# Kernel optimization log

Measured on AMD Instinct MI355X. Metric: run time of the kernel, lower is better.

Reference implementation:

```python
import jax, jax.numpy as jnp
import numpy as np

B, C, H, W = 4, 256, 128, 128
D = 256            # attention hidden_dim (== C, so no output_proj)
HID = 1024         # mlp hidden = int(C * 4.0)
EPS = 1e-5


def setup_inputs() -> dict:
    key = jax.random.key(0)
    ks = jax.random.split(key, 16)
    s = 0.02
    return {
        "x": jax.random.normal(ks[0], (B, C, H, W), jnp.float32),
        "wq": jax.random.normal(ks[1], (C, D), jnp.float32) * s,
        "bq": jnp.zeros((D,), jnp.float32),
        "wk": jax.random.normal(ks[2], (C, D), jnp.float32) * s,
        "bk": jnp.zeros((D,), jnp.float32),
        "wv": jax.random.normal(ks[3], (C, D), jnp.float32) * s,
        "bv": jnp.zeros((D,), jnp.float32),
        "ln1_g": jnp.ones((C,), jnp.float32),
        "ln1_b": jnp.zeros((C,), jnp.float32),
        "ln2_g": jnp.ones((C,), jnp.float32),
        "ln2_b": jnp.zeros((C,), jnp.float32),
        "fc1_w": jax.random.normal(ks[4], (C, HID), jnp.float32) * s,
        "fc1_b": jnp.zeros((HID,), jnp.float32),
        "fc2_w": jax.random.normal(ks[5], (HID, C), jnp.float32) * s,
        "fc2_b": jnp.zeros((C,), jnp.float32),
    }


def _layernorm(x, g, b):
    m = jnp.mean(x, axis=-1, keepdims=True)
    v = jnp.mean(jnp.square(x - m), axis=-1, keepdims=True)
    return (x - m) * jax.lax.rsqrt(v + EPS) * g + b


def _neighborhoods(t):
    # t: [B,H,W,D] -> [B,H,W,9,D] 3x3 neighborhoods, zero-padded at borders
    tp = jnp.pad(t, ((0, 0), (1, 1), (1, 1), (0, 0)))
    h, w = t.shape[1], t.shape[2]
    return jnp.stack(
        [tp[:, dy:dy + h, dx:dx + w, :] for dy in range(3) for dx in range(3)],
        axis=3,
    )


def _valid_mask(h, w):
    # [H,W,9] bool: which of the 9 neighbors are inside the grid
    ys = jnp.arange(h)[:, None] * jnp.ones((1, w), jnp.int32)
    xs = jnp.arange(w)[None, :] * jnp.ones((h, 1), jnp.int32)
    top, bot = ys > 0, ys < h - 1
    lef, rig = xs > 0, xs < w - 1
    ones = jnp.ones((h, w), bool)
    return jnp.stack(
        [top & lef, top, top & rig, lef, ones, rig, bot & lef, bot, bot & rig],
        axis=-1,
    )


def reference(x, wq, bq, wk, bk, wv, bv, ln1_g, ln1_b, ln2_g, ln2_b,
              fc1_w, fc1_b, fc2_w, fc2_b):
    b_, c_, h_, w_ = x.shape
    xc = jnp.transpose(x, (0, 2, 3, 1))                    # [B,H,W,C]
    n1 = _layernorm(xc, ln1_g, ln1_b)
    q = n1 @ wq + bq                                       # [B,H,W,D]
    k = n1 @ wk + bk
    v = n1 @ wv + bv
    kn = _neighborhoods(k)                                  # [B,H,W,9,D]
    vn = _neighborhoods(v)
    scores = jnp.einsum('bhwd,bhwnd->bhwn', q, kn) / jnp.sqrt(jnp.float32(q.shape[-1]))
    mask = _valid_mask(h_, w_)                               # [H,W,9]
    scores = jnp.where(mask, scores, jnp.float32(-1e9))
    weights = jax.nn.softmax(scores, axis=-1)
    attn = jnp.einsum('bhwn,bhwnd->bhwd', weights, vn)       # [B,H,W,D]
    x1 = xc + attn                                           # residual 1
    n2 = _layernorm(x1, ln2_g, ln2_b)
    mlp = jax.nn.gelu(n2 @ fc1_w + fc1_b, approximate=False) @ fc2_w + fc2_b
    out = x1 + mlp
    return jnp.transpose(out, (0, 3, 1, 2))                  # [B,C,H,W]
```

## Files before the change

### kernel.cpp

```cpp
#include <hip/hip_runtime.h>
#include <hip/hip_bf16.h>
#include <math.h>

#define NPIX  65536
#define CCH   256
#define HWSZ  16384
#define WIDTH 128
#define HID   1024

typedef unsigned short u16;
typedef __bf16 bf16x8 __attribute__((ext_vector_type(8)));
typedef float  floatx4 __attribute__((ext_vector_type(4)));

__device__ __forceinline__ float bf2f(u16 u) {
  union { unsigned int i; float f; } c; c.i = ((unsigned int)u) << 16; return c.f;
}
__device__ __forceinline__ float bflo(unsigned int u) {
  union { unsigned int i; float f; } c; c.i = u << 16; return c.f;
}
__device__ __forceinline__ float bfhi(unsigned int u) {
  union { unsigned int i; float f; } c; c.i = u & 0xffff0000u; return c.f;
}
__device__ __forceinline__ u16 f2bf(float f) {
  union { float f; unsigned int i; } c; c.f = f;
  unsigned int x = c.i;
  x += 0x7fffu + ((x >> 16) & 1u);
  return (u16)(x >> 16);
}
__device__ __forceinline__ unsigned int packbf(float lo, float hi) {
  return ((unsigned int)f2bf(hi) << 16) | (unsigned int)f2bf(lo);
}
__device__ __forceinline__ float fast_rcp(float x) {
  float r; asm("v_rcp_f32 %0, %1" : "=v"(r) : "v"(x)); return r;
}
__device__ __forceinline__ float fast_exp2(float x) {
  float r; asm("v_exp_f32 %0, %1" : "=v"(r) : "v"(x)); return r;
}
__device__ __forceinline__ float gelu_fast(float x) {
  const float u = x * x;
  const float s = x * fmaf(0.1029432f, u, 2.3022082f);
  const float e = fast_exp2(-s);
  return x * fast_rcp(1.0f + e);
}

__device__ __forceinline__ void async16(const void* g, void* l) {
  __builtin_amdgcn_global_load_lds(
      (const __attribute__((address_space(1))) void*)g,
      (__attribute__((address_space(3))) void*)l, 16, 0, 0);
}

__global__ __launch_bounds__(256) void wfrag_kernel(
    const float* __restrict__ src, u16* __restrict__ dst, int N, int K) {
  const int tid = threadIdx.x;
  const int u = blockIdx.x * 4 + (tid >> 6);
  const int lane = tid & 63, quad = lane >> 4, l16 = lane & 15;
  const int K32 = K >> 5;
  const int g = u / K32, kb = u - g * K32;
  const int n = g * 16 + l16;
  const int k0 = kb * 32 + quad * 8;
  u16 tmp[8];
#pragma unroll
  for (int e = 0; e < 8; e++) tmp[e] = f2bf(src[(size_t)(k0 + e) * N + n]);
  *(bf16x8*)(dst + ((size_t)u * 64 + lane) * 8) = *(bf16x8*)tmp;
}

__global__ __launch_bounds__(256) void concat_bias_kernel(
    const float* __restrict__ bq, const float* __restrict__ bk,
    const float* __restrict__ bv, float* __restrict__ dst) {
  const int i = blockIdx.x * 256 + threadIdx.x;
  if (i < 256) dst[i] = bq[i];
  else if (i < 512) dst[i] = bk[i - 256];
  else if (i < 768) dst[i] = bv[i - 512];
}

__global__ __launch_bounds__(256) void ln1_kernel(
    const float* __restrict__ x, const float* __restrict__ g,
    const float* __restrict__ bb, u16* __restrict__ n1) {
  __shared__ float sx[32][257];
  __shared__ float sred[16][32];
  __shared__ float sm[32], sr[32];
  const int tx = threadIdx.x;
  const int p0 = blockIdx.x * 32;
  {
    const int pix = tx & 31, cpart = tx >> 5;
    const int p = p0 + pix;
    const int b = p >> 14, hw = p & (HWSZ - 1);
    const float* xb = x + ((size_t)b * CCH) * HWSZ + hw;
    float s = 0.f, s2 = 0.f;
#pragma unroll 4
    for (int i = 0; i < 32; i++) {
      const int c = cpart * 32 + i;
      const float v = xb[(size_t)c * HWSZ];
      sx[pix][c] = v;
      s += v; s2 += v * v;
    }
    sred[cpart][pix] = s; sred[8 + cpart][pix] = s2;
  }
  __syncthreads();
  if (tx < 32) {
    float s = 0.f, s2 = 0.f;
#pragma unroll
    for (int j = 0; j < 8; j++) { s += sred[j][tx]; s2 += sred[8 + j][tx]; }
    const float m = s * (1.0f / 256.0f);
    const float var = s2 * (1.0f / 256.0f) - m * m;
    sm[tx] = m; sr[tx] = rsqrtf(var + 1e-5f);
  }
  __syncthreads();
  const float gc = g[tx], bc = bb[tx];
#pragma unroll 4
  for (int i = 0; i < 32; i++) {
    const float v = (sx[i][tx] - sm[i]) * sr[i] * gc + bc;
    n1[(size_t)(p0 + i) * CCH + tx] = f2bf(v);
  }
}

__global__ __launch_bounds__(256) void res_ln2_kernel(
    const float* __restrict__ x, const u16* __restrict__ attn,
    const float* __restrict__ g, const float* __restrict__ bb,
    float* __restrict__ x1, u16* __restrict__ n2) {
  __shared__ float sx[32][257];
  __shared__ float sred[16][32];
  __shared__ float sm[32], sr[32];
  const int tx = threadIdx.x;
  const int p0 = blockIdx.x * 32;
  {
    const int pix = tx & 31, cpart = tx >> 5;
    const int p = p0 + pix;
    const int b = p >> 14, hw = p & (HWSZ - 1);
    const float* xb = x + ((size_t)b * CCH) * HWSZ + hw;
#pragma unroll 4
    for (int i = 0; i < 32; i++) {
      const int c = cpart * 32 + i;
      sx[pix][c] = xb[(size_t)c * HWSZ];
    }
  }
  __syncthreads();
#pragma unroll 4
  for (int i = 0; i < 32; i++) {
    const float v = sx[i][tx] + bf2f(attn[(size_t)(p0 + i) * CCH + tx]);
    sx[i][tx] = v;
    x1[(size_t)(p0 + i) * CCH + tx] = v;
  }
  __syncthreads();
  {
    const int pix = tx & 31, cpart = tx >> 5;
    float s = 0.f, s2 = 0.f;
#pragma unroll 4
    for (int i = 0; i < 32; i++) {
      const float v = sx[pix][cpart * 32 + i];
      s += v; s2 += v * v;
    }
    sred[cpart][pix] = s; sred[8 + cpart][pix] = s2;
  }
  __syncthreads();
  if (tx < 32) {
    float s = 0.f, s2 = 0.f;
#pragma unroll
    for (int j = 0; j < 8; j++) { s += sred[j][tx]; s2 += sred[8 + j][tx]; }
    const float m = s * (1.0f / 256.0f);
    const float var = s2 * (1.0f / 256.0f) - m * m;
    sm[tx] = m; sr[tx] = rsqrtf(var + 1e-5f);
  }
  __syncthreads();
  const float gc = g[tx], bc = bb[tx];
#pragma unroll 4
  for (int i = 0; i < 32; i++) {
    const float v = (sx[i][tx] - sm[i]) * sr[i] * gc + bc;
    n2[(size_t)(p0 + i) * CCH + tx] = f2bf(v);
  }
}

__global__ __launch_bounds__(256) void attn_kernel(
    const u16* __restrict__ qkv, u16* __restrict__ attn) {
  const int tid = threadIdx.x;
  const int wave = tid >> 6, lane = tid & 63;
  const int p = blockIdx.x * 4 + wave;
  const int hw = p & (HWSZ - 1);
  const int hh = hw >> 7, ww = hw & (WIDTH - 1);
  const u16* rowp = qkv + (size_t)p * 768 + lane * 4;
  const uint2 qr = *(const uint2*)rowp;
  const float qf0 = bflo(qr.x), qf1 = bfhi(qr.x);
  const float qf2 = bflo(qr.y), qf3 = bfhi(qr.y);
  float sc[9];
#pragma unroll
  for (int n = 0; n < 9; n++) {
    const int dy = n / 3 - 1, dx = n % 3 - 1;
    const int y = hh + dy, x2 = ww + dx;
    float s = -1e30f;
    if (y >= 0 && y < 128 && x2 >= 0 && x2 < 128) {
      const uint2 kr = *(const uint2*)(rowp + 256 + (dy * WIDTH + dx) * 768);
      float d = qf0 * bflo(kr.x) + qf1 * bfhi(kr.x)
              + qf2 * bflo(kr.y) + qf3 * bfhi(kr.y);
#pragma unroll
      for (int o = 32; o >= 1; o >>= 1) d += __shfl_xor(d, o, 64);
      s = d * 0.0625f;
    }
    sc[n] = s;
  }
  float mx = sc[0];
#pragma unroll
  for (int n = 1; n < 9; n++) mx = fmaxf(mx, sc[n]);
  float wgt[9], wsum = 0.f;
#pragma unroll
  for (int n = 0; n < 9; n++) { wgt[n] = __expf(sc[n] - mx); wsum += wgt[n]; }
  const float inv = 1.0f / wsum;
  float a0 = 0.f, a1 = 0.f, a2 = 0.f, a3 = 0.f;
#pragma unroll
  for (int n = 0; n < 9; n++) {
    const int dy = n / 3 - 1, dx = n % 3 - 1;
    const int y = hh + dy, x2 = ww + dx;
    if (y >= 0 && y < 128 && x2 >= 0 && x2 < 128) {
      const uint2 vr = *(const uint2*)(rowp + 512 + (dy * WIDTH + dx) * 768);
      const float wn = wgt[n] * inv;
      a0 += wn * bflo(vr.x); a1 += wn * bfhi(vr.x);
      a2 += wn * bflo(vr.y); a3 += wn * bfhi(vr.y);
    }
  }
  uint2 o;
  o.x = ((unsigned int)f2bf(a1) << 16) | (unsigned int)f2bf(a0);
  o.y = ((unsigned int)f2bf(a3) << 16) | (unsigned int)f2bf(a2);
  *(uint2*)(attn + (size_t)p * CCH + lane * 4) = o;
}

template <int NCH, int NST, int EPI>
__global__ __launch_bounds__(256, 3) void gemm_blds(
    const u16* __restrict__ A, const u16* __restrict__ wf,
    const float* __restrict__ bias, u16* __restrict__ outb) {
  __shared__ u16 sB[2][16384];
  const int tid  = threadIdx.x;
  const int wave = tid >> 6, lane = tid & 63;
  const int quad = lane >> 4, l16 = lane & 15;
  const int m0 = blockIdx.x * 128 + wave * 32;

  const u16* aRow = A + (size_t)(m0 + l16) * CCH + quad * 8;
  bf16x8 afr[2][8];
#pragma unroll
  for (int mi = 0; mi < 2; mi++)
#pragma unroll
    for (int ks = 0; ks < 8; ks++)
      afr[mi][ks] = *(const bf16x8*)(aRow + (size_t)mi * 16 * CCH + ks * 32);

  u16* rowPtr0 = outb + (size_t)(m0 + l16) * NST;
  u16* rowPtr1 = rowPtr0 + (size_t)16 * NST;

  auto stage = [&](int ch, int buf) {
    const u16* g = wf + (size_t)ch * 16384;
#pragma unroll
    for (int i = 0; i < 8; i++)
      async16(g + i * 2048 + tid * 8, &sB[buf][i * 2048 + tid * 8]);
  };

  stage(0, 0);
#pragma unroll 1
  for (int ch = 0; ch < NCH; ++ch) {
    __syncthreads();
    if (ch + 1 < NCH) stage(ch + 1, (ch + 1) & 1);
    const u16* sb = sB[ch & 1];
    floatx4 acc[2][4];
#pragma unroll
    for (int mi = 0; mi < 2; mi++)
#pragma unroll
      for (int gi = 0; gi < 4; gi++) acc[mi][gi] = (floatx4){0.f, 0.f, 0.f, 0.f};
#pragma unroll
    for (int ks = 0; ks < 8; ks++) {
      bf16x8 bfr[4];
#pragma unroll
      for (int gi = 0; gi < 4; gi++)
        bfr[gi] = *(const bf16x8*)&sb[(gi * 8 + ks) * 512 + lane * 8];
#pragma unroll
      for (int mi = 0; mi < 2; mi++)
#pragma unroll
        for (int gi = 0; gi < 4; gi++)
          acc[mi][gi] = __builtin_amdgcn_mfma_f32_16x16x32_bf16(
              bfr[gi], afr[mi][ks], acc[mi][gi], 0, 0, 0);
    }
#pragma unroll
    for (int gi = 0; gi < 4; gi++) {
      const int colb = ch * 64 + gi * 16 + quad * 4;
      const floatx4 bs4 = *(const floatx4*)&bias[colb];
#pragma unroll
      for (int mi = 0; mi < 2; mi++) {
        float v[4];
#pragma unroll
        for (int r = 0; r < 4; r++) {
          float val = acc[mi][gi][r] + bs4[r];
          if constexpr (EPI == 1) val = gelu_fast(val);
          v[r] = val;
        }
        uint2 w;
        w.x = packbf(v[0], v[1]);
        w.y = packbf(v[2], v[3]);
        *(uint2*)((mi == 0 ? rowPtr0 : rowPtr1) + colb) = w;
      }
    }
  }
}

__global__ __launch_bounds__(256, 2) void fc2_kernel(
    const u16* __restrict__ h, const u16* __restrict__ f2F,
    const float* __restrict__ bias, const float* __restrict__ x1,
    float* __restrict__ out) {
  __shared__ u16 sA[2][8192];
  const int tid  = threadIdx.x;
  const int wave = tid >> 6, lane = tid & 63;
  const int quad = lane >> 4, l16 = lane & 15;
  const int bx = blockIdx.x;
  const int mblk = (bx >> 1) * 128;
  const int nb = bx & 1;
  const int wgi = (wave >> 1) * 4;
  const int mloc = (wave & 1) * 64;

  auto stageA = [&](int kc, int buf) {
#pragma unroll
    for (int i = 0; i < 4; i++) {
      const int s = i * 256 + tid;
      const int row = s >> 3;
      const int cb = (s & 7) ^ (row & 7);
      async16(h + (size_t)(mblk + row) * HID + kc * 64 + cb * 8,
              &sA[buf][s * 8]);
    }
  };

  const u16* bBase = f2F + (((size_t)(nb * 8 + wgi)) << 14) + lane * 8;
  auto loadB = [&](bf16x8 (&b)[2][4], int kc) {
#pragma unroll
    for (int ks = 0; ks < 2; ks++)
#pragma unroll
      for (int gi = 0; gi < 4; gi++)
        b[ks][gi] = *(const bf16x8*)(bBase + (((size_t)gi * 32 + kc * 2 + ks) << 9));
  };

  floatx4 acc[4][4];
#pragma unroll
  for (int mi = 0; mi < 4; mi++)
#pragma unroll
    for (int gi = 0; gi < 4; gi++) acc[mi][gi] = (floatx4){0.f, 0.f, 0.f, 0.f};

  auto compute = [&](const u16* sa, bf16x8 (&bfr)[2][4]) {
#pragma unroll
    for (int ks = 0; ks < 2; ks++) {
      bf16x8 afr[4];
#pragma unroll
      for (int mi = 0; mi < 4; mi++) {
        const int lr = mloc + mi * 16 + l16;
        const int ck = (ks * 32 + quad * 8) ^ ((l16 & 7) * 8);
        afr[mi] = *(const bf16x8*)&sa[lr * 64 + ck];
      }
#pragma unroll
      for (int mi = 0; mi < 4; mi++)
#pragma unroll
        for (int gi = 0; gi < 4; gi++)
          acc[mi][gi] = __builtin_amdgcn_mfma_f32_16x16x32_bf16(
              afr[mi], bfr[ks][gi], acc[mi][gi], 0, 0, 0);
    }
  };

  bf16x8 b0[2][4], b1[2][4];
  stageA(0, 0);
  loadB(b0, 0);
#pragma unroll 1
  for (int kc = 0; kc < 16; kc += 2) {
    __syncthreads();
    loadB(b1, kc + 1);
    stageA(kc + 1, 1);
    compute(sA[0], b0);
    __syncthreads();
    if (kc + 2 < 16) { loadB(b0, kc + 2); stageA(kc + 2, 0); }
    compute(sA[1], b1);
  }

  const int m0 = mblk + mloc;
#pragma unroll
  for (int mi = 0; mi < 4; mi++)
#pragma unroll
    for (int gi = 0; gi < 4; gi++) {
      const int col = nb * 128 + (wgi + gi) * 16 + l16;
      const float bs = bias[col];
      const int row0 = m0 + mi * 16 + quad * 4;
      floatx4 vv;
#pragma unroll
      for (int r = 0; r < 4; r++)
        vv[r] = acc[mi][gi][r] + bs + x1[(size_t)(row0 + r) * CCH + col];
      *(floatx4*)&out[((size_t)((row0 >> 14) * CCH + col)) * HWSZ + (row0 & (HWSZ - 1))] = vv;
    }
}

extern "C" void kernel_launch(void* const* d_in, const int* in_sizes, int n_in,
                              void* d_out, int out_size, void* d_ws, size_t ws_size,
                              hipStream_t stream) {
  const float* x    = (const float*)d_in[0];
  const float* wq   = (const float*)d_in[1];
  const float* bq   = (const float*)d_in[2];
  const float* wk   = (const float*)d_in[3];
  const float* bk   = (const float*)d_in[4];
  const float* wv   = (const float*)d_in[5];
  const float* bv   = (const float*)d_in[6];
  const float* ln1g = (const float*)d_in[7];
  const float* ln1b = (const float*)d_in[8];
  const float* ln2g = (const float*)d_in[9];
  const float* ln2b = (const float*)d_in[10];
  const float* fc1w = (const float*)d_in[11];
  const float* fc1b = (const float*)d_in[12];
  const float* fc2w = (const float*)d_in[13];
  const float* fc2b = (const float*)d_in[14];
  float* out = (float*)d_out;

  char* ws = (char*)d_ws;
  const size_t MB = (size_t)1 << 20;
  float* x1   = (float*)(ws);
  u16* qkv    = (u16*)(ws + 64 * MB);
  u16* hbuf   = (u16*)(ws + 64 * MB);
  u16* n1     = (u16*)(ws + 160 * MB);
  u16* attnb  = n1;
  u16* n2     = (u16*)(ws + 192 * MB);
  u16* wqkvF  = (u16*)(ws + 224 * MB);
  u16* f1F    = wqkvF + 768 * 256;
  u16* f2F    = f1F + 1024 * 256;
  float* bqkv = (float*)(f2F + 256 * 1024);

  dim3 blk(256);
  wfrag_kernel<<<dim3(32),  blk, 0, stream>>>(wq,   wqkvF,          256, 256);
  wfrag_kernel<<<dim3(32),  blk, 0, stream>>>(wk,   wqkvF + 65536,  256, 256);
  wfrag_kernel<<<dim3(32),  blk, 0, stream>>>(wv,   wqkvF + 131072, 256, 256);
  wfrag_kernel<<<dim3(128), blk, 0, stream>>>(fc1w, f1F, 1024, 256);
  wfrag_kernel<<<dim3(128), blk, 0, stream>>>(fc2w, f2F, 256, 1024);
  concat_bias_kernel<<<dim3(3), blk, 0, stream>>>(bq, bk, bv, bqkv);

  ln1_kernel<<<NPIX / 32, blk, 0, stream>>>(x, ln1g, ln1b, n1);

  gemm_blds<12, 768, 0><<<dim3(NPIX / 128), blk, 0, stream>>>(n1, wqkvF, bqkv, qkv);

  attn_kernel<<<NPIX / 4, blk, 0, stream>>>(qkv, attnb);

  res_ln2_kernel<<<NPIX / 32, blk, 0, stream>>>(x, attnb, ln2g, ln2b, x1, n2);

  gemm_blds<16, 1024, 1><<<dim3(NPIX / 128), blk, 0, stream>>>(n2, f1F, fc1b, hbuf);

  fc2_kernel<<<dim3((NPIX / 128) * 2), blk, 0, stream>>>(hbuf, f2F, fc2b, x1, out);
}
```

Before: 445.5 us.

## Deepen async prefetch with fine-grained vmcnt waits in FC kernels

The FC1-style kernel replaces __syncthreads with a partial vmcnt wait plus a raw barrier, and hoists the bias loads ahead of the MMA loop. The fc2 kernel moves from a double-buffered to a four-buffered shared A tile, staging two K chunks ahead. Its full block syncs become targeted vmcnt waits with scheduling barriers, so global loads overlap more of the MFMA compute. This doubles fc2 LDS usage to 64KB, which could lower occupancy under launch_bounds(256,2). The hand-counted vmcnt values must match the number of outstanding loads exactly, or the kernels will read stale data.

Result: no change. 449.3 us (+0.9%).

```diff
diff --git a/kernel.cpp b/kernel.cpp
--- a/kernel.cpp
+++ b/kernel.cpp
@@ -253,8 +253,16 @@
   stage(0, 0);
 #pragma unroll 1
   for (int ch = 0; ch < NCH; ++ch) {
-    __syncthreads();
+    if (ch == 0) asm volatile("s_waitcnt vmcnt(0)" ::: "memory");
+    else         asm volatile("s_waitcnt vmcnt(8)" ::: "memory");
+    __builtin_amdgcn_s_barrier();
+    __builtin_amdgcn_sched_barrier(0);
+    floatx4 bs4pre[4];
+#pragma unroll
+    for (int gi = 0; gi < 4; gi++)
+      bs4pre[gi] = *(const floatx4*)&bias[ch * 64 + gi * 16 + quad * 4];
     if (ch + 1 < NCH) stage(ch + 1, (ch + 1) & 1);
+    __builtin_amdgcn_sched_barrier(0);
     const u16* sb = sB[ch & 1];
     floatx4 acc[2][4];
 #pragma unroll
@@ -277,7 +285,7 @@
 #pragma unroll
     for (int gi = 0; gi < 4; gi++) {
       const int colb = ch * 64 + gi * 16 + quad * 4;
-      const floatx4 bs4 = *(const floatx4*)&bias[colb];
+      const floatx4 bs4 = bs4pre[gi];
 #pragma unroll
       for (int mi = 0; mi < 2; mi++) {
         float v[4];
@@ -300,7 +308,7 @@
     const u16* __restrict__ h, const u16* __restrict__ f2F,
     const float* __restrict__ bias, const float* __restrict__ x1,
     float* __restrict__ out) {
-  __shared__ u16 sA[2][8192];
+  __shared__ u16 sA[4][8192];
   const int tid  = threadIdx.x;
   const int wave = tid >> 6, lane = tid & 63;
   const int quad = lane >> 4, l16 = lane & 15;
@@ -358,15 +366,24 @@
   bf16x8 b0[2][4], b1[2][4];
   stageA(0, 0);
   loadB(b0, 0);
+  stageA(1, 1);
 #pragma unroll 1
   for (int kc = 0; kc < 16; kc += 2) {
-    __syncthreads();
+    asm volatile("s_waitcnt vmcnt(4)" ::: "memory");
+    __builtin_amdgcn_s_barrier();
+    __builtin_amdgcn_sched_barrier(0);
     loadB(b1, kc + 1);
-    stageA(kc + 1, 1);
-    compute(sA[0], b0);
-    __syncthreads();
-    if (kc + 2 < 16) { loadB(b0, kc + 2); stageA(kc + 2, 0); }
-    compute(sA[1], b1);
+    if (kc + 2 < 16) stageA(kc + 2, (kc + 2) & 3);
+    __builtin_amdgcn_sched_barrier(0);
+    compute(sA[kc & 3], b0);
+    if (kc == 14) asm volatile("s_waitcnt vmcnt(0)" ::: "memory");
+    else          asm volatile("s_waitcnt vmcnt(4)" ::: "memory");
+    __builtin_amdgcn_s_barrier();
+    __builtin_amdgcn_sched_barrier(0);
+    if (kc + 2 < 16) loadB(b0, kc + 2);
+    if (kc + 3 < 16) stageA(kc + 3, (kc + 3) & 3);
+    __builtin_amdgcn_sched_barrier(0);
+    compute(sA[(kc + 1) & 3], b1);
   }
 
   const int m0 = mblk + mloc;
```
